# Performance work log

Hardware: AMD Instinct MI355X
Metric: run time of the kernel (lower is better)

The kernel has to match this reference:

```python
import jax, jax.numpy as jnp
import numpy as np

N, M, D, H = 2048, 32, 768, 512
TEMP, THRESH, EPS = 0.05, 1e-4, 1e-6


def setup_inputs() -> dict:
    key = jax.random.key(0)
    ks = jax.random.split(key, 7)
    q = jax.random.normal(ks[0], (D,), dtype=jnp.float32)
    X = jax.random.normal(ks[1], (N, D), dtype=jnp.float32)
    C_init = jax.random.normal(ks[2], (M, D), dtype=jnp.float32)
    # nn.Linear default init: U(-1/sqrt(fan_in), 1/sqrt(fan_in))
    s1 = 1.0 / np.sqrt(5 * D)
    W1 = jax.random.uniform(ks[3], (5 * D, H), jnp.float32, -s1, s1)
    b1 = jax.random.uniform(ks[4], (H,), jnp.float32, -s1, s1)
    s2 = 1.0 / np.sqrt(H)
    W2 = jax.random.uniform(ks[5], (H, 1), jnp.float32, -s2, s2)
    b2 = jax.random.uniform(ks[6], (1,), jnp.float32, -s2, s2)
    return {"q": q, "X": X, "C_init": C_init, "W1": W1, "b1": b1, "W2": W2, "b2": b2}


def _learned_dist(q, x, y, W1, b1, W2, b2):
    # pairwise features: for each (i,j): [x_i, y_j, |x_i-y_j|, |x_i-q|, |y_j-q|]
    n, m, d = x.shape[0], y.shape[0], x.shape[1]
    xb = jnp.broadcast_to(x[:, None, :], (n, m, d))
    yb = jnp.broadcast_to(y[None, :, :], (n, m, d))
    feat = jnp.concatenate(
        [xb, yb, jnp.abs(xb - yb), jnp.abs(xb - q), jnp.abs(yb - q)], axis=-1
    )  # (n, m, 5d)
    h = jax.nn.relu(jnp.einsum("nmf,fh->nmh", feat, W1) + b1)
    return jax.nn.sigmoid(jnp.einsum("nmh,ho->nmo", h, W2)[..., 0] + b2[0])  # (n, m)


def reference(q, X, C_init, W1, b1, W2, b2):
    d = -_learned_dist(q, X, C_init, W1, b1, W2, b2)          # (N, M)
    a = jax.nn.softmax(d / TEMP, axis=1)                       # (N, M)
    a_sum = jnp.sum(a, axis=0) + EPS                           # (M,)
    C_new = (a.T @ X) / a_sum[:, None]                         # (M, D)
    # Torch loop always recomputes with C_init, so it runs at most once and
    # returns C_new iff the initial diff exceeds the threshold, else C_init.
    diff = jnp.sum(jnp.abs(C_new - C_init))                    # L1 norm
    C_final = jnp.where(diff > THRESH, C_new, C_init)
    return (C_final, a)
```

## Files before the change

kernel.cpp:

```cpp
#include <hip/hip_runtime.h>
#include <hip/hip_fp16.h>
#include <math.h>

#define NN 2048
#define MM 32
#define DD 768
#define HH 512
#define KT 24
#define WBLK ((size_t)KT * 16384)
constexpr float TEMP = 0.05f;
constexpr float THRESH = 1e-4f;
constexpr float EPS = 1e-6f;

typedef _Float16 halfx8 __attribute__((ext_vector_type(8)));
typedef float floatx4 __attribute__((ext_vector_type(4)));

__device__ __forceinline__ halfx8 habs8(halfx8 a, halfx8 b) {
    halfx8 d = a - b;
    union { halfx8 h; unsigned int u[4]; } x;
    x.h = d;
    #pragma unroll
    for (int e = 0; e < 4; ++e) x.u[e] &= 0x7FFF7FFFu;
    return x.h;
}

__global__ __launch_bounds__(256) void prep_kernel(
    const float* __restrict__ X, const float* __restrict__ W1,
    _Float16* __restrict__ Xf, _Float16* __restrict__ Wf)
{
    __shared__ float Wt[32 * 512];
    const int t = threadIdx.x;
    if (blockIdx.x < 192) {
        #pragma unroll
        for (int p = 0; p < 4; ++p) {
            int u = blockIdx.x * 1024 + p * 256 + t;
            int it = u / 1536;
            int rem = u - it * 1536;
            int kt = rem >> 6;
            int lane = rem & 63;
            int row = it * 16 + (lane & 15);
            int kb = kt * 32 + (lane >> 4) * 8;
            const float* xp = X + (size_t)row * DD + kb;
            float4 xa = *(const float4*)xp;
            float4 xb = *(const float4*)(xp + 4);
            halfx8 v;
            v[0] = (_Float16)xa.x; v[1] = (_Float16)xa.y;
            v[2] = (_Float16)xa.z; v[3] = (_Float16)xa.w;
            v[4] = (_Float16)xb.x; v[5] = (_Float16)xb.y;
            v[6] = (_Float16)xb.z; v[7] = (_Float16)xb.w;
            *(halfx8*)(Xf + (size_t)u * 8) = v;
        }
    } else {
        const int b = blockIdx.x - 192;
        const int wb = b / 24;
        const int kt = b % 24;
        const int rowbase = wb * 768;
        #pragma unroll
        for (int rep = 0; rep < 16; ++rep) {
            int idx = rep * 256 + t;
            int row = idx >> 7;
            int c4 = (idx & 127) * 4;
            *(float4*)&Wt[row * 512 + c4] =
                *(const float4*)(W1 + (size_t)(rowbase + kt * 32 + row) * HH + c4);
        }
        __syncthreads();
        #pragma unroll
        for (int g = 0; g < 8; ++g) {
            halfx8 v;
            #pragma unroll
            for (int jj = 0; jj < 8; ++jj) {
                int o = t * 64 + g * 8 + jj;
                int nt = o >> 9;
                int l  = (o >> 3) & 63;
                int j  = o & 7;
                int k  = ((l >> 4) << 3) + j;
                int n  = nt * 16 + (l & 15);
                v[jj] = (_Float16)Wt[k * 512 + n];
            }
            *(halfx8*)(Wf + (size_t)wb * WBLK + (size_t)kt * 16384 + t * 64 + g * 8) = v;
        }
    }
}

__global__ __launch_bounds__(512, 2) void build_A_kernel(
    const float* __restrict__ q, const _Float16* __restrict__ Xf,
    const _Float16* __restrict__ Wf, _Float16* __restrict__ Arowh)
{
    __shared__ _Float16 qh[DD];
    const int t = threadIdx.x;
    const int lane = t & 63;
    const int cg = t >> 6;
    const int q4 = lane >> 4;
    const int l16 = lane & 15;
    const int hs = blockIdx.x;
    const int by = blockIdx.y;
    const int nt = hs * 8 + cg;

    for (int d = t; d < DD; d += 512) qh[d] = (_Float16)q[d];
    __syncthreads();

    const _Float16* ap0 = Xf + ((size_t)((by * 2 + 0) * 24) * 64 + lane) * 8;
    const _Float16* ap1 = Xf + ((size_t)((by * 2 + 1) * 24) * 64 + lane) * 8;
    const _Float16* bpA = Wf + (size_t)nt * 512 + (size_t)lane * 8;
    const _Float16* bpD = Wf + 3 * WBLK + (size_t)nt * 512 + (size_t)lane * 8;

    floatx4 acc[2];
    acc[0] = (floatx4)0.f; acc[1] = (floatx4)0.f;

    halfx8 Afc[2], Bac, Bdc, Afn[2], Ban, Bdn;
    Afc[0] = *(const halfx8*)ap0;
    Afc[1] = *(const halfx8*)ap1;
    Bac = *(const halfx8*)bpA;
    Bdc = *(const halfx8*)bpD;

    for (int kt = 0; kt < KT; ++kt) {
        if (kt < KT - 1) {
            Afn[0] = *(const halfx8*)(ap0 + (kt + 1) * 512);
            Afn[1] = *(const halfx8*)(ap1 + (kt + 1) * 512);
            Ban = *(const halfx8*)(bpA + (size_t)(kt + 1) * 16384);
            Bdn = *(const halfx8*)(bpD + (size_t)(kt + 1) * 16384);
        }
        halfx8 qf = *(halfx8*)&qh[kt * 32 + q4 * 8];
        #pragma unroll
        for (int rt = 0; rt < 2; ++rt) {
            halfx8 Zd = habs8(Afc[rt], qf);
            acc[rt] = __builtin_amdgcn_mfma_f32_16x16x32_f16(Afc[rt], Bac, acc[rt], 0, 0, 0);
            acc[rt] = __builtin_amdgcn_mfma_f32_16x16x32_f16(Zd, Bdc, acc[rt], 0, 0, 0);
        }
        Afc[0] = Afn[0]; Afc[1] = Afn[1]; Bac = Ban; Bdc = Bdn;
    }
    #pragma unroll
    for (int rt = 0; rt < 2; ++rt)
        #pragma unroll
        for (int reg = 0; reg < 4; ++reg) {
            int i = by * 32 + rt * 16 + q4 * 4 + reg;
            int h = nt * 16 + l16;
            Arowh[(size_t)i * HH + h] = (_Float16)acc[rt][reg];
        }
}

__global__ __launch_bounds__(512) void build_B_kernel(
    const float* __restrict__ C_init, const float* __restrict__ q,
    const _Float16* __restrict__ Wf, const float* __restrict__ b1,
    float* __restrict__ Brow)
{
    __shared__ _Float16 yh[32 * 776];
    __shared__ _Float16 qh[DD];
    __shared__ floatx4 Bred[8][2][64];
    const int t = threadIdx.x;
    const int lane = t & 63;
    const int wv = t >> 6;
    const int q4 = lane >> 4;
    const int l16 = lane & 15;
    const int nt = blockIdx.x;

    for (int r = 0; r < 32; ++r)
        for (int d = t; d < DD; d += 512)
            yh[r * 776 + d] = (_Float16)C_init[(size_t)r * DD + d];
    for (int d = t; d < DD; d += 512) qh[d] = (_Float16)q[d];
    __syncthreads();

    const _Float16* Wb = Wf + 1 * WBLK;
    const _Float16* We = Wf + 4 * WBLK;

    floatx4 acc[2];
    acc[0] = (floatx4)0.f; acc[1] = (floatx4)0.f;

    #pragma unroll
    for (int r = 0; r < 3; ++r) {
        int kt = wv + r * 8;
        halfx8 qf = *(halfx8*)&qh[kt * 32 + q4 * 8];
        size_t wo = (size_t)kt * 16384 + (size_t)nt * 512 + (size_t)lane * 8;
        halfx8 Bb = *(const halfx8*)(Wb + wo);
        halfx8 Be = *(const halfx8*)(We + wo);
        #pragma unroll
        for (int rt = 0; rt < 2; ++rt) {
            halfx8 Ab = *(halfx8*)&yh[(rt * 16 + l16) * 776 + kt * 32 + q4 * 8];
            halfx8 Ze = habs8(Ab, qf);
            acc[rt] = __builtin_amdgcn_mfma_f32_16x16x32_f16(Ab, Bb, acc[rt], 0, 0, 0);
            acc[rt] = __builtin_amdgcn_mfma_f32_16x16x32_f16(Ze, Be, acc[rt], 0, 0, 0);
        }
    }
    Bred[wv][0][lane] = acc[0];
    Bred[wv][1][lane] = acc[1];
    __syncthreads();
    if (wv < 2) {
        int rt = wv;
        floatx4 s = Bred[0][rt][lane];
        #pragma unroll
        for (int w = 1; w < 8; ++w) s += Bred[w][rt][lane];
        #pragma unroll
        for (int reg = 0; reg < 4; ++reg) {
            int j = rt * 16 + q4 * 4 + reg;
            int h = nt * 16 + l16;
            Brow[(size_t)j * HH + h] = s[reg] + b1[h];
        }
    }
}

__global__ __launch_bounds__(512, 2) void pairwise_kernel(
    const _Float16* __restrict__ Xf, const _Float16* __restrict__ Wf,
    const float* __restrict__ Y,
    const _Float16* __restrict__ Arowh, const float* __restrict__ Brow,
    const float* __restrict__ W2, float* __restrict__ Spart)
{
    __shared__ _Float16 yh[4 * DD];
    __shared__ float Sred[4][4][64];
    const int t = threadIdx.x;
    const int lane = t & 63;
    const int wv = t >> 6;
    const int wr = wv >> 2;
    const int cq = wv & 3;
    const int q4 = lane >> 4;
    const int l16 = lane & 15;
    const int i0 = blockIdx.x * 64;
    const int hs = blockIdx.y & 1;
    const int j0 = (blockIdx.y >> 1) * 4;

    for (int d = t; d < DD; d += 512) {
        #pragma unroll
        for (int jj = 0; jj < 4; ++jj)
            yh[jj * DD + d] = (_Float16)Y[(size_t)(j0 + jj) * DD + d];
    }
    __syncthreads();

    const _Float16* Wc = Wf + 2 * WBLK;
    const _Float16* ap0 = Xf + ((size_t)((blockIdx.x * 4 + wr * 2 + 0) * 24) * 64 + lane) * 8;
    const _Float16* ap1 = Xf + ((size_t)((blockIdx.x * 4 + wr * 2 + 1) * 24) * 64 + lane) * 8;
    const _Float16* bp = Wc + (size_t)(hs * 16 + cq * 4) * 512 + (size_t)lane * 8;

    floatx4 acc[4][2][4];
    #pragma unroll
    for (int jj = 0; jj < 4; ++jj)
        #pragma unroll
        for (int rt = 0; rt < 2; ++rt)
            #pragma unroll
            for (int ct = 0; ct < 4; ++ct) acc[jj][rt][ct] = (floatx4)0.f;

    halfx8 Afc[2], Bfc[4], Afn[2], Bfn[4];
    Afc[0] = *(const halfx8*)ap0;
    Afc[1] = *(const halfx8*)ap1;
    #pragma unroll
    for (int ct = 0; ct < 4; ++ct) Bfc[ct] = *(const halfx8*)(bp + ct * 512);

    for (int kt = 0; kt < KT; ++kt) {
        if (kt < KT - 1) {
            Afn[0] = *(const halfx8*)(ap0 + (kt + 1) * 512);
            Afn[1] = *(const halfx8*)(ap1 + (kt + 1) * 512);
            #pragma unroll
            for (int ct = 0; ct < 4; ++ct)
                Bfn[ct] = *(const halfx8*)(bp + (size_t)(kt + 1) * 16384 + ct * 512);
        }
        halfx8 hv[4];
        #pragma unroll
        for (int jj = 0; jj < 4; ++jj)
            hv[jj] = *(halfx8*)&yh[jj * DD + kt * 32 + q4 * 8];
        #pragma unroll
        for (int jj = 0; jj < 4; ++jj) {
            halfx8 Zf0 = habs8(Afc[0], hv[jj]);
            halfx8 Zf1 = habs8(Afc[1], hv[jj]);
            #pragma unroll
            for (int ct = 0; ct < 4; ++ct) {
                acc[jj][0][ct] = __builtin_amdgcn_mfma_f32_16x16x32_f16(Zf0, Bfc[ct], acc[jj][0][ct], 0, 0, 0);
                acc[jj][1][ct] = __builtin_amdgcn_mfma_f32_16x16x32_f16(Zf1, Bfc[ct], acc[jj][1][ct], 0, 0, 0);
            }
        }
        Afc[0] = Afn[0]; Afc[1] = Afn[1];
        #pragma unroll
        for (int ct = 0; ct < 4; ++ct) Bfc[ct] = Bfn[ct];
    }

    float w2v[4], bv[4][4];
    #pragma unroll
    for (int ct = 0; ct < 4; ++ct) {
        int h = hs * 256 + cq * 64 + ct * 16 + l16;
        w2v[ct] = W2[h];
        #pragma unroll
        for (int jj = 0; jj < 4; ++jj)
            bv[jj][ct] = Brow[(size_t)(j0 + jj) * HH + h];
    }
    #pragma unroll
    for (int rt = 0; rt < 2; ++rt)
        #pragma unroll
        for (int reg = 0; reg < 4; ++reg) {
            int row = wr * 32 + rt * 16 + q4 * 4 + reg;
            const _Float16* ap = Arowh + (size_t)(i0 + row) * HH + hs * 256 + cq * 64 + l16;
            float av[4];
            #pragma unroll
            for (int ct = 0; ct < 4; ++ct) av[ct] = (float)ap[ct * 16];
            #pragma unroll
            for (int jj = 0; jj < 4; ++jj) {
                float s = 0.f;
                #pragma unroll
                for (int ct = 0; ct < 4; ++ct) {
                    float pre = acc[jj][rt][ct][reg] + av[ct] + bv[jj][ct];
                    s = fmaf(fmaxf(pre, 0.f), w2v[ct], s);
                }
                s += __shfl_xor(s, 1, 64);
                s += __shfl_xor(s, 2, 64);
                s += __shfl_xor(s, 4, 64);
                s += __shfl_xor(s, 8, 64);
                if (l16 == 0) Sred[jj][cq][row] = s;
            }
        }
    __syncthreads();
    if (t < 256) {
        int row = t & 63, jj = t >> 6;
        float s = Sred[jj][0][row] + Sred[jj][1][row] + Sred[jj][2][row] + Sred[jj][3][row];
        Spart[((size_t)hs * NN + (i0 + row)) * MM + j0 + jj] = s;
    }
}

__global__ __launch_bounds__(256) void softmax_kernel(
    const float* __restrict__ Spart, const float* __restrict__ b2,
    float* __restrict__ a_out)
{
    const int t = threadIdx.x;
    const int j = t & 31, r = t >> 5;
    const int i = blockIdx.x * 8 + r;
    const float b2v = b2[0];
    float s = Spart[(size_t)i * MM + j] + Spart[(size_t)(NN + i) * MM + j];
    float sig = 1.f / (1.f + expf(-(s + b2v)));
    float l = -sig * (1.0f / TEMP);
    float m = l;
    #pragma unroll
    for (int off = 16; off >= 1; off >>= 1) m = fmaxf(m, __shfl_xor(m, off, 32));
    float e = expf(l - m);
    float sum = e;
    #pragma unroll
    for (int off = 16; off >= 1; off >>= 1) sum += __shfl_xor(sum, off, 32);
    a_out[(size_t)i * MM + j] = e / sum;
}

__global__ __launch_bounds__(256) void cnew_part_kernel(
    const float* __restrict__ a, const float* __restrict__ X,
    float* __restrict__ Cpart, float* __restrict__ Apart)
{
    const int t = threadIdx.x;
    const int dl = t & 63, jg = t >> 6;
    const int d = blockIdx.x * 64 + dl;
    const int ic = blockIdx.y;
    const int j0 = jg * 8;
    float acc[8] = {};
    float asum[8] = {};
    const int ibase = ic * 64;
    #pragma unroll 4
    for (int ii = 0; ii < 64; ++ii) {
        int i = ibase + ii;
        float xv = X[(size_t)i * DD + d];
        float4 a0 = *(const float4*)(a + (size_t)i * MM + j0);
        float4 a1 = *(const float4*)(a + (size_t)i * MM + j0 + 4);
        acc[0] = fmaf(a0.x, xv, acc[0]); asum[0] += a0.x;
        acc[1] = fmaf(a0.y, xv, acc[1]); asum[1] += a0.y;
        acc[2] = fmaf(a0.z, xv, acc[2]); asum[2] += a0.z;
        acc[3] = fmaf(a0.w, xv, acc[3]); asum[3] += a0.w;
        acc[4] = fmaf(a1.x, xv, acc[4]); asum[4] += a1.x;
        acc[5] = fmaf(a1.y, xv, acc[5]); asum[5] += a1.y;
        acc[6] = fmaf(a1.z, xv, acc[6]); asum[6] += a1.z;
        acc[7] = fmaf(a1.w, xv, acc[7]); asum[7] += a1.w;
    }
    #pragma unroll
    for (int jj = 0; jj < 8; ++jj)
        Cpart[((size_t)ic * MM + j0 + jj) * DD + d] = acc[jj];
    if (blockIdx.x == 0 && dl == 0)
        #pragma unroll
        for (int jj = 0; jj < 8; ++jj)
            Apart[ic * MM + j0 + jj] = asum[jj];
}

__global__ __launch_bounds__(256) void merge_kernel(
    const float* __restrict__ Cpart, const float* __restrict__ Apart,
    const float* __restrict__ C_init, float* __restrict__ C_new,
    float* __restrict__ Dpart)
{
    __shared__ float wred[4];
    const int j = blockIdx.x;
    const int t = threadIdx.x;
    float asum = 0.f;
    #pragma unroll
    for (int ic = 0; ic < 32; ++ic) asum += Apart[ic * MM + j];
    const float inv = 1.f / (asum + EPS);
    float ad = 0.f;
    #pragma unroll
    for (int dc = 0; dc < 3; ++dc) {
        int d = dc * 256 + t;
        float s = 0.f;
        #pragma unroll
        for (int ic = 0; ic < 32; ++ic)
            s += Cpart[((size_t)ic * MM + j) * DD + d];
        float c = s * inv;
        C_new[(size_t)j * DD + d] = c;
        ad += fabsf(c - C_init[(size_t)j * DD + d]);
    }
    #pragma unroll
    for (int off = 32; off >= 1; off >>= 1) ad += __shfl_xor(ad, off, 64);
    if ((t & 63) == 0) wred[t >> 6] = ad;
    __syncthreads();
    if (t == 0) Dpart[j] = wred[0] + wred[1] + wred[2] + wred[3];
}

__global__ __launch_bounds__(256) void select_kernel(
    const float* __restrict__ C_new, const float* __restrict__ C_init,
    const float* __restrict__ Dpart, float* __restrict__ out)
{
    __shared__ float ds[32];
    const int t = threadIdx.x;
    if (t < 32) ds[t] = Dpart[t];
    __syncthreads();
    float dv = 0.f;
    #pragma unroll
    for (int jj = 0; jj < 32; ++jj) dv += ds[jj];
    const int k = blockIdx.x * 256 + t;
    out[k] = (dv > THRESH) ? C_new[k] : C_init[k];
}

extern "C" void kernel_launch(void* const* d_in, const int* in_sizes, int n_in,
                              void* d_out, int out_size, void* d_ws, size_t ws_size,
                              hipStream_t stream)
{
    const float* q      = (const float*)d_in[0];
    const float* X      = (const float*)d_in[1];
    const float* C_init = (const float*)d_in[2];
    const float* W1     = (const float*)d_in[3];
    const float* b1     = (const float*)d_in[4];
    const float* W2     = (const float*)d_in[5];
    const float* b2     = (const float*)d_in[6];

    float* out_C = (float*)d_out;
    float* out_a = (float*)d_out + (size_t)MM * DD;

    float* ws = (float*)d_ws;
    _Float16* Wf    = (_Float16*)ws;
    _Float16* Xf    = (_Float16*)(ws + 983040);
    _Float16* Arowh = (_Float16*)(ws + 1769472);
    float* Brow  = ws + 2293760;
    float* Spart = ws + 2310144;
    float* Cpart = ws + 2441216;
    float* Apart = ws + 3227648;
    float* Dpart = ws + 3228672;
    float* Cn    = ws + 3228704;

    prep_kernel<<<312, 256, 0, stream>>>(X, W1, Xf, Wf);
    build_A_kernel<<<dim3(4, 64), 512, 0, stream>>>(q, Xf, Wf, Arowh);
    build_B_kernel<<<32, 512, 0, stream>>>(C_init, q, Wf, b1, Brow);
    pairwise_kernel<<<dim3(32, 16), 512, 0, stream>>>(Xf, Wf, C_init, Arowh, Brow, W2, Spart);
    softmax_kernel<<<256, 256, 0, stream>>>(Spart, b2, out_a);
    cnew_part_kernel<<<dim3(12, 32), 256, 0, stream>>>(out_a, X, Cpart, Apart);
    merge_kernel<<<32, 256, 0, stream>>>(Cpart, Apart, C_init, Cn, Dpart);
    select_kernel<<<96, 256, 0, stream>>>(Cn, C_init, Dpart, out_C);
}
```

Measured before the change: 192.3 us.

## Fuse build kernels, halve pairwise j-tile, fuse softmax into C update

Measured after the change: 182.7 us. -5.0%, faster.

```diff
diff --git a/kernel.cpp b/kernel.cpp
--- a/kernel.cpp
+++ b/kernel.cpp
@@ -82,130 +82,125 @@
     }
 }
 
-__global__ __launch_bounds__(512, 2) void build_A_kernel(
-    const float* __restrict__ q, const _Float16* __restrict__ Xf,
-    const _Float16* __restrict__ Wf, _Float16* __restrict__ Arowh)
-{
-    __shared__ _Float16 qh[DD];
-    const int t = threadIdx.x;
-    const int lane = t & 63;
-    const int cg = t >> 6;
-    const int q4 = lane >> 4;
-    const int l16 = lane & 15;
-    const int hs = blockIdx.x;
-    const int by = blockIdx.y;
-    const int nt = hs * 8 + cg;
-
-    for (int d = t; d < DD; d += 512) qh[d] = (_Float16)q[d];
-    __syncthreads();
-
-    const _Float16* ap0 = Xf + ((size_t)((by * 2 + 0) * 24) * 64 + lane) * 8;
-    const _Float16* ap1 = Xf + ((size_t)((by * 2 + 1) * 24) * 64 + lane) * 8;
-    const _Float16* bpA = Wf + (size_t)nt * 512 + (size_t)lane * 8;
-    const _Float16* bpD = Wf + 3 * WBLK + (size_t)nt * 512 + (size_t)lane * 8;
-
-    floatx4 acc[2];
-    acc[0] = (floatx4)0.f; acc[1] = (floatx4)0.f;
-
-    halfx8 Afc[2], Bac, Bdc, Afn[2], Ban, Bdn;
-    Afc[0] = *(const halfx8*)ap0;
-    Afc[1] = *(const halfx8*)ap1;
-    Bac = *(const halfx8*)bpA;
-    Bdc = *(const halfx8*)bpD;
-
-    for (int kt = 0; kt < KT; ++kt) {
-        if (kt < KT - 1) {
-            Afn[0] = *(const halfx8*)(ap0 + (kt + 1) * 512);
-            Afn[1] = *(const halfx8*)(ap1 + (kt + 1) * 512);
-            Ban = *(const halfx8*)(bpA + (size_t)(kt + 1) * 16384);
-            Bdn = *(const halfx8*)(bpD + (size_t)(kt + 1) * 16384);
-        }
-        halfx8 qf = *(halfx8*)&qh[kt * 32 + q4 * 8];
-        #pragma unroll
-        for (int rt = 0; rt < 2; ++rt) {
-            halfx8 Zd = habs8(Afc[rt], qf);
-            acc[rt] = __builtin_amdgcn_mfma_f32_16x16x32_f16(Afc[rt], Bac, acc[rt], 0, 0, 0);
-            acc[rt] = __builtin_amdgcn_mfma_f32_16x16x32_f16(Zd, Bdc, acc[rt], 0, 0, 0);
-        }
-        Afc[0] = Afn[0]; Afc[1] = Afn[1]; Bac = Ban; Bdc = Bdn;
-    }
-    #pragma unroll
-    for (int rt = 0; rt < 2; ++rt)
-        #pragma unroll
-        for (int reg = 0; reg < 4; ++reg) {
-            int i = by * 32 + rt * 16 + q4 * 4 + reg;
-            int h = nt * 16 + l16;
-            Arowh[(size_t)i * HH + h] = (_Float16)acc[rt][reg];
-        }
-}
-
-__global__ __launch_bounds__(512) void build_B_kernel(
-    const float* __restrict__ C_init, const float* __restrict__ q,
-    const _Float16* __restrict__ Wf, const float* __restrict__ b1,
-    float* __restrict__ Brow)
-{
-    __shared__ _Float16 yh[32 * 776];
-    __shared__ _Float16 qh[DD];
-    __shared__ floatx4 Bred[8][2][64];
+__global__ __launch_bounds__(512, 2) void build_AB_kernel(
+    const float* __restrict__ q, const float* __restrict__ C_init,
+    const _Float16* __restrict__ Xf, const _Float16* __restrict__ Wf,
+    const float* __restrict__ b1,
+    _Float16* __restrict__ Arowh, float* __restrict__ Brow)
+{
+    __shared__ __align__(16) char smem[67584];
     const int t = threadIdx.x;
     const int lane = t & 63;
     const int wv = t >> 6;
     const int q4 = lane >> 4;
     const int l16 = lane & 15;
-    const int nt = blockIdx.x;
-
-    for (int r = 0; r < 32; ++r)
-        for (int d = t; d < DD; d += 512)
-            yh[r * 776 + d] = (_Float16)C_init[(size_t)r * DD + d];
-    for (int d = t; d < DD; d += 512) qh[d] = (_Float16)q[d];
-    __syncthreads();
-
-    const _Float16* Wb = Wf + 1 * WBLK;
-    const _Float16* We = Wf + 4 * WBLK;
-
-    floatx4 acc[2];
-    acc[0] = (floatx4)0.f; acc[1] = (floatx4)0.f;
-
-    #pragma unroll
-    for (int r = 0; r < 3; ++r) {
-        int kt = wv + r * 8;
-        halfx8 qf = *(halfx8*)&qh[kt * 32 + q4 * 8];
-        size_t wo = (size_t)kt * 16384 + (size_t)nt * 512 + (size_t)lane * 8;
-        halfx8 Bb = *(const halfx8*)(Wb + wo);
-        halfx8 Be = *(const halfx8*)(We + wo);
-        #pragma unroll
-        for (int rt = 0; rt < 2; ++rt) {
-            halfx8 Ab = *(halfx8*)&yh[(rt * 16 + l16) * 776 + kt * 32 + q4 * 8];
-            halfx8 Ze = habs8(Ab, qf);
-            acc[rt] = __builtin_amdgcn_mfma_f32_16x16x32_f16(Ab, Bb, acc[rt], 0, 0, 0);
-            acc[rt] = __builtin_amdgcn_mfma_f32_16x16x32_f16(Ze, Be, acc[rt], 0, 0, 0);
-        }
-    }
-    Bred[wv][0][lane] = acc[0];
-    Bred[wv][1][lane] = acc[1];
-    __syncthreads();
-    if (wv < 2) {
-        int rt = wv;
-        floatx4 s = Bred[0][rt][lane];
-        #pragma unroll
-        for (int w = 1; w < 8; ++w) s += Bred[w][rt][lane];
-        #pragma unroll
-        for (int reg = 0; reg < 4; ++reg) {
-            int j = rt * 16 + q4 * 4 + reg;
-            int h = nt * 16 + l16;
-            Brow[(size_t)j * HH + h] = s[reg] + b1[h];
-        }
-    }
-}
-
-__global__ __launch_bounds__(512, 2) void pairwise_kernel(
+
+    if (blockIdx.x < 256) {
+        _Float16* qh = (_Float16*)smem;
+        const int hs = blockIdx.x & 3;
+        const int by = blockIdx.x >> 2;
+        const int nt = hs * 8 + wv;
+
+        for (int d = t; d < DD; d += 512) qh[d] = (_Float16)q[d];
+        __syncthreads();
+
+        const _Float16* ap0 = Xf + ((size_t)((by * 2 + 0) * 24) * 64 + lane) * 8;
+        const _Float16* ap1 = Xf + ((size_t)((by * 2 + 1) * 24) * 64 + lane) * 8;
+        const _Float16* bpA = Wf + (size_t)nt * 512 + (size_t)lane * 8;
+        const _Float16* bpD = Wf + 3 * WBLK + (size_t)nt * 512 + (size_t)lane * 8;
+
+        floatx4 acc[2];
+        acc[0] = (floatx4)0.f; acc[1] = (floatx4)0.f;
+
+        halfx8 Afc[2], Bac, Bdc, Afn[2], Ban, Bdn;
+        Afc[0] = *(const halfx8*)ap0;
+        Afc[1] = *(const halfx8*)ap1;
+        Bac = *(const halfx8*)bpA;
+        Bdc = *(const halfx8*)bpD;
+
+        for (int kt = 0; kt < KT; ++kt) {
+            if (kt < KT - 1) {
+                Afn[0] = *(const halfx8*)(ap0 + (kt + 1) * 512);
+                Afn[1] = *(const halfx8*)(ap1 + (kt + 1) * 512);
+                Ban = *(const halfx8*)(bpA + (size_t)(kt + 1) * 16384);
+                Bdn = *(const halfx8*)(bpD + (size_t)(kt + 1) * 16384);
+            }
+            halfx8 qf = *(halfx8*)&qh[kt * 32 + q4 * 8];
+            #pragma unroll
+            for (int rt = 0; rt < 2; ++rt) {
+                halfx8 Zd = habs8(Afc[rt], qf);
+                acc[rt] = __builtin_amdgcn_mfma_f32_16x16x32_f16(Afc[rt], Bac, acc[rt], 0, 0, 0);
+                acc[rt] = __builtin_amdgcn_mfma_f32_16x16x32_f16(Zd, Bdc, acc[rt], 0, 0, 0);
+            }
+            Afc[0] = Afn[0]; Afc[1] = Afn[1]; Bac = Ban; Bdc = Bdn;
+        }
+        #pragma unroll
+        for (int rt = 0; rt < 2; ++rt)
+            #pragma unroll
+            for (int reg = 0; reg < 4; ++reg) {
+                int i = by * 32 + rt * 16 + q4 * 4 + reg;
+                int h = nt * 16 + l16;
+                Arowh[(size_t)i * HH + h] = (_Float16)acc[rt][reg];
+            }
+    } else {
+        _Float16* yh = (_Float16*)smem;
+        _Float16* qh = yh + 32 * 776;
+        floatx4* Bred = (floatx4*)(smem + (32 * 776 + DD) * 2);
+        const int nt = blockIdx.x - 256;
+
+        for (int r = 0; r < 32; ++r)
+            for (int d = t; d < DD; d += 512)
+                yh[r * 776 + d] = (_Float16)C_init[(size_t)r * DD + d];
+        for (int d = t; d < DD; d += 512) qh[d] = (_Float16)q[d];
+        __syncthreads();
+
+        const _Float16* Wb = Wf + 1 * WBLK;
+        const _Float16* We = Wf + 4 * WBLK;
+
+        floatx4 acc[2];
+        acc[0] = (floatx4)0.f; acc[1] = (floatx4)0.f;
+
+        #pragma unroll
+        for (int r = 0; r < 3; ++r) {
+            int kt = wv + r * 8;
+            halfx8 qf = *(halfx8*)&qh[kt * 32 + q4 * 8];
+            size_t wo = (size_t)kt * 16384 + (size_t)nt * 512 + (size_t)lane * 8;
+            halfx8 Bb = *(const halfx8*)(Wb + wo);
+            halfx8 Be = *(const halfx8*)(We + wo);
+            #pragma unroll
+            for (int rt = 0; rt < 2; ++rt) {
+                halfx8 Ab = *(halfx8*)&yh[(rt * 16 + l16) * 776 + kt * 32 + q4 * 8];
+                halfx8 Ze = habs8(Ab, qf);
+                acc[rt] = __builtin_amdgcn_mfma_f32_16x16x32_f16(Ab, Bb, acc[rt], 0, 0, 0);
+                acc[rt] = __builtin_amdgcn_mfma_f32_16x16x32_f16(Ze, Be, acc[rt], 0, 0, 0);
+            }
+        }
+        Bred[(wv * 2 + 0) * 64 + lane] = acc[0];
+        Bred[(wv * 2 + 1) * 64 + lane] = acc[1];
+        __syncthreads();
+        if (wv < 2) {
+            int rt = wv;
+            floatx4 s = Bred[rt * 64 + lane];
+            #pragma unroll
+            for (int w = 1; w < 8; ++w) s += Bred[(w * 2 + rt) * 64 + lane];
+            #pragma unroll
+            for (int reg = 0; reg < 4; ++reg) {
+                int j = rt * 16 + q4 * 4 + reg;
+                int h = nt * 16 + l16;
+                Brow[(size_t)j * HH + h] = s[reg] + b1[h];
+            }
+        }
+    }
+}
+
+__global__ __launch_bounds__(512, 4) void pairwise_kernel(
     const _Float16* __restrict__ Xf, const _Float16* __restrict__ Wf,
     const float* __restrict__ Y,
     const _Float16* __restrict__ Arowh, const float* __restrict__ Brow,
     const float* __restrict__ W2, float* __restrict__ Spart)
 {
-    __shared__ _Float16 yh[4 * DD];
-    __shared__ float Sred[4][4][64];
+    __shared__ _Float16 yh[2 * DD];
+    __shared__ float Sred[2][4][64];
     const int t = threadIdx.x;
     const int lane = t & 63;
     const int wv = t >> 6;
@@ -215,12 +210,11 @@
     const int l16 = lane & 15;
     const int i0 = blockIdx.x * 64;
     const int hs = blockIdx.y & 1;
-    const int j0 = (blockIdx.y >> 1) * 4;
+    const int j0 = (blockIdx.y >> 1) * 2;
 
     for (int d = t; d < DD; d += 512) {
-        #pragma unroll
-        for (int jj = 0; jj < 4; ++jj)
-            yh[jj * DD + d] = (_Float16)Y[(size_t)(j0 + jj) * DD + d];
+        yh[d]      = (_Float16)Y[(size_t)j0 * DD + d];
+        yh[DD + d] = (_Float16)Y[(size_t)(j0 + 1) * DD + d];
     }
     __syncthreads();
 
@@ -229,55 +223,42 @@
     const _Float16* ap1 = Xf + ((size_t)((blockIdx.x * 4 + wr * 2 + 1) * 24) * 64 + lane) * 8;
     const _Float16* bp = Wc + (size_t)(hs * 16 + cq * 4) * 512 + (size_t)lane * 8;
 
-    floatx4 acc[4][2][4];
-    #pragma unroll
-    for (int jj = 0; jj < 4; ++jj)
+    floatx4 acc[2][2][4];
+    #pragma unroll
+    for (int jj = 0; jj < 2; ++jj)
         #pragma unroll
         for (int rt = 0; rt < 2; ++rt)
             #pragma unroll
             for (int ct = 0; ct < 4; ++ct) acc[jj][rt][ct] = (floatx4)0.f;
 
-    halfx8 Afc[2], Bfc[4], Afn[2], Bfn[4];
-    Afc[0] = *(const halfx8*)ap0;
-    Afc[1] = *(const halfx8*)ap1;
-    #pragma unroll
-    for (int ct = 0; ct < 4; ++ct) Bfc[ct] = *(const halfx8*)(bp + ct * 512);
-
     for (int kt = 0; kt < KT; ++kt) {
-        if (kt < KT - 1) {
-            Afn[0] = *(const halfx8*)(ap0 + (kt + 1) * 512);
-            Afn[1] = *(const halfx8*)(ap1 + (kt + 1) * 512);
-            #pragma unroll
-            for (int ct = 0; ct < 4; ++ct)
-                Bfn[ct] = *(const halfx8*)(bp + (size_t)(kt + 1) * 16384 + ct * 512);
-        }
-        halfx8 hv[4];
-        #pragma unroll
-        for (int jj = 0; jj < 4; ++jj)
-            hv[jj] = *(halfx8*)&yh[jj * DD + kt * 32 + q4 * 8];
-        #pragma unroll
-        for (int jj = 0; jj < 4; ++jj) {
-            halfx8 Zf0 = habs8(Afc[0], hv[jj]);
-            halfx8 Zf1 = habs8(Afc[1], hv[jj]);
-            #pragma unroll
-            for (int ct = 0; ct < 4; ++ct) {
-                acc[jj][0][ct] = __builtin_amdgcn_mfma_f32_16x16x32_f16(Zf0, Bfc[ct], acc[jj][0][ct], 0, 0, 0);
-                acc[jj][1][ct] = __builtin_amdgcn_mfma_f32_16x16x32_f16(Zf1, Bfc[ct], acc[jj][1][ct], 0, 0, 0);
-            }
-        }
-        Afc[0] = Afn[0]; Afc[1] = Afn[1];
-        #pragma unroll
-        for (int ct = 0; ct < 4; ++ct) Bfc[ct] = Bfn[ct];
-    }
-
-    float w2v[4], bv[4][4];
+        halfx8 Af[2], Bf[4], hv[2];
+        Af[0] = *(const halfx8*)(ap0 + kt * 512);
+        Af[1] = *(const halfx8*)(ap1 + kt * 512);
+        #pragma unroll
+        for (int ct = 0; ct < 4; ++ct)
+            Bf[ct] = *(const halfx8*)(bp + (size_t)kt * 16384 + ct * 512);
+        hv[0] = *(halfx8*)&yh[kt * 32 + q4 * 8];
+        hv[1] = *(halfx8*)&yh[DD + kt * 32 + q4 * 8];
+        #pragma unroll
+        for (int jj = 0; jj < 2; ++jj)
+            #pragma unroll
+            for (int rt = 0; rt < 2; ++rt) {
+                halfx8 Zf = habs8(Af[rt], hv[jj]);
+                #pragma unroll
+                for (int ct = 0; ct < 4; ++ct)
+                    acc[jj][rt][ct] = __builtin_amdgcn_mfma_f32_16x16x32_f16(
+                        Zf, Bf[ct], acc[jj][rt][ct], 0, 0, 0);
+            }
+    }
+
+    float w2v[4], bv[2][4];
     #pragma unroll
     for (int ct = 0; ct < 4; ++ct) {
         int h = hs * 256 + cq * 64 + ct * 16 + l16;
         w2v[ct] = W2[h];
-        #pragma unroll
-        for (int jj = 0; jj < 4; ++jj)
-            bv[jj][ct] = Brow[(size_t)(j0 + jj) * HH + h];
+        bv[0][ct] = Brow[(size_t)j0 * HH + h];
+        bv[1][ct] = Brow[(size_t)(j0 + 1) * HH + h];
     }
     #pragma unroll
     for (int rt = 0; rt < 2; ++rt)
@@ -289,7 +270,7 @@
             #pragma unroll
             for (int ct = 0; ct < 4; ++ct) av[ct] = (float)ap[ct * 16];
             #pragma unroll
-            for (int jj = 0; jj < 4; ++jj) {
+            for (int jj = 0; jj < 2; ++jj) {
                 float s = 0.f;
                 #pragma unroll
                 for (int ct = 0; ct < 4; ++ct) {
@@ -304,52 +285,62 @@
             }
         }
     __syncthreads();
-    if (t < 256) {
+    if (t < 128) {
         int row = t & 63, jj = t >> 6;
         float s = Sred[jj][0][row] + Sred[jj][1][row] + Sred[jj][2][row] + Sred[jj][3][row];
         Spart[((size_t)hs * NN + (i0 + row)) * MM + j0 + jj] = s;
     }
 }
 
-__global__ __launch_bounds__(256) void softmax_kernel(
+__global__ __launch_bounds__(256) void cnew_sm_kernel(
     const float* __restrict__ Spart, const float* __restrict__ b2,
-    float* __restrict__ a_out)
-{
-    const int t = threadIdx.x;
-    const int j = t & 31, r = t >> 5;
-    const int i = blockIdx.x * 8 + r;
+    const float* __restrict__ X,
+    float* __restrict__ a_out, float* __restrict__ Cpart,
+    float* __restrict__ Apart)
+{
+    __shared__ float a_s[64][36];
+    const int t = threadIdx.x;
+    const int dc = blockIdx.x;
+    const int ic = blockIdx.y;
+    const int ibase = ic * 64;
     const float b2v = b2[0];
-    float s = Spart[(size_t)i * MM + j] + Spart[(size_t)(NN + i) * MM + j];
-    float sig = 1.f / (1.f + expf(-(s + b2v)));
-    float l = -sig * (1.0f / TEMP);
-    float m = l;
-    #pragma unroll
-    for (int off = 16; off >= 1; off >>= 1) m = fmaxf(m, __shfl_xor(m, off, 32));
-    float e = expf(l - m);
-    float sum = e;
-    #pragma unroll
-    for (int off = 16; off >= 1; off >>= 1) sum += __shfl_xor(sum, off, 32);
-    a_out[(size_t)i * MM + j] = e / sum;
-}
-
-__global__ __launch_bounds__(256) void cnew_part_kernel(
-    const float* __restrict__ a, const float* __restrict__ X,
-    float* __restrict__ Cpart, float* __restrict__ Apart)
-{
-    const int t = threadIdx.x;
+
+    {
+        const int j = t & 31, r = t >> 5;
+        #pragma unroll
+        for (int rb = 0; rb < 8; ++rb) {
+            int il = rb * 8 + r;
+            int i = ibase + il;
+            float s = Spart[(size_t)i * MM + j] + Spart[(size_t)(NN + i) * MM + j];
+            float sig = 1.f / (1.f + expf(-(s + b2v)));
+            float l = -sig * (1.0f / TEMP);
+            float m = l;
+            #pragma unroll
+            for (int off = 16; off >= 1; off >>= 1) m = fmaxf(m, __shfl_xor(m, off, 32));
+            float e = expf(l - m);
+            float sum = e;
+            #pragma unroll
+            for (int off = 16; off >= 1; off >>= 1) sum += __shfl_xor(sum, off, 32);
+            a_s[il][j] = e / sum;
+        }
+    }
+    __syncthreads();
+    if (dc == 0) {
+        #pragma unroll
+        for (int p = 0; p < 8; ++p) {
+            int k = p * 256 + t;
+            a_out[(size_t)(ibase + (k >> 5)) * MM + (k & 31)] = a_s[k >> 5][k & 31];
+        }
+    }
     const int dl = t & 63, jg = t >> 6;
-    const int d = blockIdx.x * 64 + dl;
-    const int ic = blockIdx.y;
-    const int j0 = jg * 8;
+    const int d = dc * 64 + dl;
     float acc[8] = {};
     float asum[8] = {};
-    const int ibase = ic * 64;
     #pragma unroll 4
     for (int ii = 0; ii < 64; ++ii) {
-        int i = ibase + ii;
-        float xv = X[(size_t)i * DD + d];
-        float4 a0 = *(const float4*)(a + (size_t)i * MM + j0);
-        float4 a1 = *(const float4*)(a + (size_t)i * MM + j0 + 4);
+        float xv = X[(size_t)(ibase + ii) * DD + d];
+        float4 a0 = *(float4*)&a_s[ii][jg * 8];
+        float4 a1 = *(float4*)&a_s[ii][jg * 8 + 4];
         acc[0] = fmaf(a0.x, xv, acc[0]); asum[0] += a0.x;
         acc[1] = fmaf(a0.y, xv, acc[1]); asum[1] += a0.y;
         acc[2] = fmaf(a0.z, xv, acc[2]); asum[2] += a0.z;
@@ -361,11 +352,11 @@
     }
     #pragma unroll
     for (int jj = 0; jj < 8; ++jj)
-        Cpart[((size_t)ic * MM + j0 + jj) * DD + d] = acc[jj];
-    if (blockIdx.x == 0 && dl == 0)
+        Cpart[((size_t)ic * MM + jg * 8 + jj) * DD + d] = acc[jj];
+    if (dc == 0 && dl == 0)
         #pragma unroll
         for (int jj = 0; jj < 8; ++jj)
-            Apart[ic * MM + j0 + jj] = asum[jj];
+            Apart[ic * MM + jg * 8 + jj] = asum[jj];
 }
 
 __global__ __launch_bounds__(256) void merge_kernel(
@@ -374,42 +365,39 @@
     float* __restrict__ Dpart)
 {
     __shared__ float wred[4];
-    const int j = blockIdx.x;
-    const int t = threadIdx.x;
+    const int dc = blockIdx.x;
+    const int j = blockIdx.y;
+    const int t = threadIdx.x;
+    const int d = dc * 256 + t;
     float asum = 0.f;
     #pragma unroll
     for (int ic = 0; ic < 32; ++ic) asum += Apart[ic * MM + j];
     const float inv = 1.f / (asum + EPS);
-    float ad = 0.f;
-    #pragma unroll
-    for (int dc = 0; dc < 3; ++dc) {
-        int d = dc * 256 + t;
-        float s = 0.f;
-        #pragma unroll
-        for (int ic = 0; ic < 32; ++ic)
-            s += Cpart[((size_t)ic * MM + j) * DD + d];
-        float c = s * inv;
-        C_new[(size_t)j * DD + d] = c;
-        ad += fabsf(c - C_init[(size_t)j * DD + d]);
-    }
+    float s = 0.f;
+    #pragma unroll
+    for (int ic = 0; ic < 32; ++ic)
+        s += Cpart[((size_t)ic * MM + j) * DD + d];
+    float c = s * inv;
+    C_new[(size_t)j * DD + d] = c;
+    float ad = fabsf(c - C_init[(size_t)j * DD + d]);
     #pragma unroll
     for (int off = 32; off >= 1; off >>= 1) ad += __shfl_xor(ad, off, 64);
     if ((t & 63) == 0) wred[t >> 6] = ad;
     __syncthreads();
-    if (t == 0) Dpart[j] = wred[0] + wred[1] + wred[2] + wred[3];
+    if (t == 0) Dpart[j * 3 + dc] = wred[0] + wred[1] + wred[2] + wred[3];
 }
 
 __global__ __launch_bounds__(256) void select_kernel(
     const float* __restrict__ C_new, const float* __restrict__ C_init,
     const float* __restrict__ Dpart, float* __restrict__ out)
 {
-    __shared__ float ds[32];
-    const int t = threadIdx.x;
-    if (t < 32) ds[t] = Dpart[t];
+    __shared__ float ds[96];
+    const int t = threadIdx.x;
+    if (t < 96) ds[t] = Dpart[t];
     __syncthreads();
     float dv = 0.f;
     #pragma unroll
-    for (int jj = 0; jj < 32; ++jj) dv += ds[jj];
+    for (int p = 0; p < 96; ++p) dv += ds[p];
     const int k = blockIdx.x * 256 + t;
     out[k] = (dv > THRESH) ? C_new[k] : C_init[k];
 }
@@ -438,14 +426,12 @@
     float* Cpart = ws + 2441216;
     float* Apart = ws + 3227648;
     float* Dpart = ws + 3228672;
-    float* Cn    = ws + 3228704;
+    float* Cn    = ws + 3228768;
 
     prep_kernel<<<312, 256, 0, stream>>>(X, W1, Xf, Wf);
-    build_A_kernel<<<dim3(4, 64), 512, 0, stream>>>(q, Xf, Wf, Arowh);
-    build_B_kernel<<<32, 512, 0, stream>>>(C_init, q, Wf, b1, Brow);
-    pairwise_kernel<<<dim3(32, 16), 512, 0, stream>>>(Xf, Wf, C_init, Arowh, Brow, W2, Spart);
-    softmax_kernel<<<256, 256, 0, stream>>>(Spart, b2, out_a);
-    cnew_part_kernel<<<dim3(12, 32), 256, 0, stream>>>(out_a, X, Cpart, Apart);
-    merge_kernel<<<32, 256, 0, stream>>>(Cpart, Apart, C_init, Cn, Dpart);
+    build_AB_kernel<<<288, 512, 0, stream>>>(q, C_init, Xf, Wf, b1, Arowh, Brow);
+    pairwise_kernel<<<dim3(32, 32), 512, 0, stream>>>(Xf, Wf, C_init, Arowh, Brow, W2, Spart);
+    cnew_sm_kernel<<<dim3(12, 32), 256, 0, stream>>>(Spart, b2, X, out_a, Cpart, Apart);
+    merge_kernel<<<dim3(3, 32), 256, 0, stream>>>(Cpart, Apart, C_init, Cn, Dpart);
     select_kernel<<<96, 256, 0, stream>>>(Cn, C_init, Dpart, out_C);
 }
```
